# Kernel tuning notes

Measured on AMD Instinct MI355X. Metric: run time of the kernel, lower is better.

The kernel has to match this reference:

```python
import jax, jax.numpy as jnp
import numpy as np
import math

N_LOC = 4096   # spatial locations
N_REP = 128    # replicates n
M_NBR = 48     # conditioning-set size m (fix_m = m_max)
SMOOTH = 1.5


def setup_inputs() -> dict:
    key = jax.random.key(0)
    k1, k2, k3, k4 = jax.random.split(key, 4)
    aug = jax.random.normal(k1, (N_REP, N_LOC, M_NBR + 1), dtype=jnp.float32)
    theta = jax.random.normal(k2, (6,), dtype=jnp.float32) * 0.1
    theta = theta.at[2].set(-2.5)  # slow scaling decay so m_max neighbors are all active
    scales = jax.random.uniform(k3, (N_LOC,), dtype=jnp.float32) + 0.5
    nug_mean = jax.random.uniform(k4, (N_LOC,), dtype=jnp.float32) + 0.5
    batch_idx = jnp.arange(N_LOC, dtype=jnp.int32)
    return {
        "augmented_response": aug,
        "theta": theta,
        "scales": scales,
        "nug_mean": nug_mean,
        "batch_idx": batch_idx,
    }


def _kernel(aug, theta, scales, nug_mean):
    m = aug.shape[-1] - 1
    # x: (n, N, m) -> (N, n, m), nan (no conditioning) -> 0
    x = aug[..., 1 : m + 1]
    x = jnp.where(jnp.isnan(x), 0.0, x)
    x = jnp.transpose(x, (1, 0, 2))  # (N, n, m)
    # scaling_fun(k) = sqrt(exp(-k * exp(theta[2]))), k = 1..m
    ks = jnp.arange(1, m + 1, dtype=aug.dtype)
    scal = jnp.sqrt(jnp.exp(-ks * jnp.exp(theta[2])))  # (m,)
    xs = x * scal  # (N, n, m)
    # linear term: per-location gram matrix (N, n, n)
    lin = jnp.einsum("Nim,Njm->Nij", xs, xs)
    # Matern-1.5 term with unit lengthscale on xs / lenScal
    len_scal = jnp.exp(theta[5]) * math.sqrt(2.0 * SMOOTH)
    xd = xs / len_scal
    sqn = jnp.sum(xd * xd, axis=-1)  # (N, n)
    sq = sqn[:, :, None] + sqn[:, None, :] - 2.0 * jnp.einsum("Nim,Njm->Nij", xd, xd)
    dist = jnp.sqrt(jnp.clip(sq, 0.0))
    sq3d = math.sqrt(3.0) * dist
    matern = (1.0 + sq3d) * jnp.exp(-sq3d)  # nu=1.5 Matern, lengthscale 1
    # sigma_fun per location: exp(log(scales) * theta[4] + theta[3])
    sigma = jnp.exp(jnp.log(scales) * theta[4] + theta[3])  # (N,)
    nonlin = (sigma**2)[:, None, None] * matern
    return (lin + nonlin) / nug_mean[:, None, None]


def reference(augmented_response, theta, scales, nug_mean, batch_idx):
    k = _kernel(augmented_response, theta, scales, nug_mean)  # (N, n, n)
    n = k.shape[-1]
    eye = jnp.eye(n, dtype=k.dtype)
    g = k + eye
    # locations with batch_idx == 0 get identity G
    g = jnp.where((batch_idx == 0)[:, None, None], eye, g)
    g_chol = jnp.linalg.cholesky(g)
    return g, g_chol
```

## Files before the change

kernel.cpp:

```cpp
#include <hip/hip_runtime.h>
#include <math.h>

#define NLOC 4096
#define NREP 128
#define MN   48
#define XSS  49

__global__ __launch_bounds__(256, 2)
void otm_fused(const float* __restrict__ aug,
               const float* __restrict__ theta,
               const float* __restrict__ scales,
               const float* __restrict__ nug_mean,
               const int*   __restrict__ batch_idx,
               float* __restrict__ out_g,
               float* __restrict__ out_l)
{
    __shared__ float xs[NREP * XSS];
    __shared__ float ldiag[NREP];
    __shared__ float scal_s[MN];
    __shared__ float wl[2][8][NREP];
    __shared__ float rs_s[NREP];

    const int loc = blockIdx.x;
    const int tid = threadIdx.x;
    const int ti  = tid >> 4;
    const int tj  = tid & 15;
    const int i0  = ti << 3;
    const int j0  = tj << 3;

    const float th2 = theta[2];
    if (tid < MN) {
        float e2 = expf(th2);
        scal_s[tid] = expf(-0.5f * (float)(tid + 1) * e2);
    }
    __syncthreads();

    for (int idx = tid; idx < NREP * MN; idx += 256) {
        int r = idx / MN;
        int c = idx - r * MN;
        float v = aug[(r * NLOC + loc) * (MN + 1) + 1 + c];
        v = (v != v) ? 0.0f : v;
        xs[r * XSS + c] = v * scal_s[c];
    }
    __syncthreads();

    if (tid < NREP) {
        float s = 0.0f;
        #pragma unroll
        for (int kk = 0; kk < MN; ++kk) {
            float v = xs[tid * XSS + kk];
            s = fmaf(v, v, s);
        }
        ldiag[tid] = s;
    }

    float acc[8][8];
    #pragma unroll
    for (int r = 0; r < 8; ++r)
        #pragma unroll
        for (int c = 0; c < 8; ++c) acc[r][c] = 0.0f;

    for (int kk = 0; kk < MN; ++kk) {
        float a[8], b[8];
        #pragma unroll
        for (int r = 0; r < 8; ++r) a[r] = xs[(i0 + r) * XSS + kk];
        #pragma unroll
        for (int c = 0; c < 8; ++c) b[c] = xs[(j0 + c) * XSS + kk];
        #pragma unroll
        for (int r = 0; r < 8; ++r)
            #pragma unroll
            for (int c = 0; c < 8; ++c)
                acc[r][c] = fmaf(a[r], b[c], acc[r][c]);
    }
    __syncthreads();

    const float s_loc   = scales[loc];
    const float th3 = theta[3], th4 = theta[4], th5 = theta[5];
    const float sig2    = expf(2.0f * fmaf(logf(s_loc), th4, th3));
    const float nug_inv = 1.0f / nug_mean[loc];
    const float ls      = expf(th5) * 1.7320508075688772f;
    const float inv_ls2 = 1.0f / (ls * ls);
    const bool  is0     = (batch_idx[loc] == 0);

    float di[8], dj[8];
    #pragma unroll
    for (int r = 0; r < 8; ++r) di[r] = ldiag[i0 + r];
    #pragma unroll
    for (int c = 0; c < 8; ++c) dj[c] = ldiag[j0 + c];

    float* gout = out_g + (size_t)loc * (NREP * NREP);
    #pragma unroll
    for (int r = 0; r < 8; ++r) {
        const int i = i0 + r;
        #pragma unroll
        for (int h = 0; h < 2; ++h) {
            float tmp[4];
            #pragma unroll
            for (int e = 0; e < 4; ++e) {
                const int c = h * 4 + e;
                const int j = j0 + c;
                float lin = acc[r][c];
                float sq  = (di[r] + dj[c] - 2.0f * lin) * inv_ls2;
                sq = fmaxf(sq, 0.0f);
                float d3  = 1.7320508075688772f * sqrtf(sq);
                float mat = (1.0f + d3) * __expf(-d3);
                float gv  = fmaf(sig2, mat, lin) * nug_inv + ((i == j) ? 1.0f : 0.0f);
                if (is0) gv = (i == j) ? 1.0f : 0.0f;
                acc[r][c] = gv;
                tmp[e] = gv;
            }
            *(float4*)(gout + (size_t)i * NREP + j0 + h * 4) =
                make_float4(tmp[0], tmp[1], tmp[2], tmp[3]);
        }
    }

    for (int p = 0; p < 16; ++p) {
        if (ti == p && tj >= p) {
            const int diagLane = ((p & 3) << 4) | p;
            float rsv[8];
            #pragma unroll
            for (int s = 0; s < 8; ++s) {
                const float piv  = __shfl(acc[s][s], diagLane);
                const float dinv = 1.0f / piv;
                rsv[s] = 1.0f / sqrtf(piv);
                #pragma unroll
                for (int sp = s + 1; sp < 8; ++sp) {
                    const float f = __shfl(acc[sp][s], diagLane) * dinv;
                    #pragma unroll
                    for (int c = 0; c < 8; ++c) {
                        if (c > s) {
                            acc[sp][c] = fmaf(-f, acc[s][c], acc[sp][c]);
                        } else if (tj > p) {
                            acc[sp][c] = fmaf(-f, acc[s][c], acc[sp][c]);
                        }
                    }
                }
            }
            #pragma unroll
            for (int s = 0; s < 8; ++s) {
                *(float4*)&wl[p & 1][s][j0] =
                    make_float4(acc[s][0] * rsv[s], acc[s][1] * rsv[s],
                                acc[s][2] * rsv[s], acc[s][3] * rsv[s]);
                *(float4*)&wl[p & 1][s][j0 + 4] =
                    make_float4(acc[s][4] * rsv[s], acc[s][5] * rsv[s],
                                acc[s][6] * rsv[s], acc[s][7] * rsv[s]);
            }
            if (tj == p) {
                #pragma unroll
                for (int s = 0; s < 8; ++s) rs_s[(p << 3) + s] = rsv[s];
            }
        }
        __syncthreads();

        if (ti > p) {
            const float (*w)[NREP] = wl[p & 1];
            if (tj > p) {
                #pragma unroll 2
                for (int s = 0; s < 8; ++s) {
                    const float4 wiA = *(const float4*)&w[s][i0];
                    const float4 wiB = *(const float4*)&w[s][i0 + 4];
                    const float4 wjA = *(const float4*)&w[s][j0];
                    const float4 wjB = *(const float4*)&w[s][j0 + 4];
                    const float wi[8] = {wiA.x, wiA.y, wiA.z, wiA.w,
                                         wiB.x, wiB.y, wiB.z, wiB.w};
                    const float wj[8] = {wjA.x, wjA.y, wjA.z, wjA.w,
                                         wjB.x, wjB.y, wjB.z, wjB.w};
                    #pragma unroll
                    for (int r = 0; r < 8; ++r)
                        #pragma unroll
                        for (int c = 0; c < 8; ++c)
                            acc[r][c] = fmaf(-wi[r], wj[c], acc[r][c]);
                }
            } else if (tj == p) {
                #pragma unroll
                for (int s = 0; s < 7; ++s) {
                    const float4 wiA = *(const float4*)&w[s][i0];
                    const float4 wiB = *(const float4*)&w[s][i0 + 4];
                    const float wi[8] = {wiA.x, wiA.y, wiA.z, wiA.w,
                                         wiB.x, wiB.y, wiB.z, wiB.w};
                    #pragma unroll
                    for (int c = 0; c < 8; ++c) {
                        if (c > s) {
                            const float wjc = w[s][j0 + c];
                            #pragma unroll
                            for (int r = 0; r < 8; ++r)
                                acc[r][c] = fmaf(-wi[r], wjc, acc[r][c]);
                        }
                    }
                }
            }
        }
    }

    float rsj[8];
    #pragma unroll
    for (int c = 0; c < 8; ++c) rsj[c] = rs_s[j0 + c];

    float* lout = out_l + (size_t)loc * (NREP * NREP);
    #pragma unroll
    for (int r = 0; r < 8; ++r) {
        const int i = i0 + r;
        #pragma unroll
        for (int h = 0; h < 2; ++h) {
            float tmp[4];
            #pragma unroll
            for (int e = 0; e < 4; ++e) {
                const int c = h * 4 + e;
                const int j = j0 + c;
                tmp[e] = (i >= j) ? acc[r][c] * rsj[c] : 0.0f;
            }
            *(float4*)(lout + (size_t)i * NREP + j0 + h * 4) =
                make_float4(tmp[0], tmp[1], tmp[2], tmp[3]);
        }
    }
}

extern "C" void kernel_launch(void* const* d_in, const int* in_sizes, int n_in,
                              void* d_out, int out_size, void* d_ws, size_t ws_size,
                              hipStream_t stream) {
    const float* aug    = (const float*)d_in[0];
    const float* theta  = (const float*)d_in[1];
    const float* scales = (const float*)d_in[2];
    const float* nug    = (const float*)d_in[3];
    const int*   bidx   = (const int*)d_in[4];
    float* g = (float*)d_out;
    float* l = g + (size_t)NLOC * NREP * NREP;
    hipLaunchKernelGGL(otm_fused, dim3(NLOC), dim3(256), 0, stream,
                       aug, theta, scales, nug, bidx, g, l);
}
```

Baseline: 1.209 ms.

## Transpose shared activations to k-major swizzled layout and raise occupancy

The scaled neighbour matrix in shared memory is stored transposed (k-major) with a padded, swizzled row index. This lets the Gram-matrix loop fetch eight rows per operand with two float4 loads instead of eight scalar loads. The Cholesky panel buffer uses the same swizzle to reduce bank conflicts. Launch bounds move from 2 to 4 blocks per CU to hide latency. The odd row stride of 141 floats leaves float4 accesses not 16-byte aligned, and the tighter register budget could cause spills.

```diff
diff --git a/kernel.cpp b/kernel.cpp
--- a/kernel.cpp
+++ b/kernel.cpp
@@ -4,9 +4,12 @@
 #define NLOC 4096
 #define NREP 128
 #define MN   48
-#define XSS  49
-
-__global__ __launch_bounds__(256, 2)
+#define XTS  141
+#define WLS  141
+
+__device__ __forceinline__ int swz(int j) { return j + ((j >> 5) << 2); }
+
+__global__ __launch_bounds__(256, 4)
 void otm_fused(const float* __restrict__ aug,
                const float* __restrict__ theta,
                const float* __restrict__ scales,
@@ -15,10 +18,10 @@
                float* __restrict__ out_g,
                float* __restrict__ out_l)
 {
-    __shared__ float xs[NREP * XSS];
+    __shared__ float xs_t[MN * XTS];
     __shared__ float ldiag[NREP];
     __shared__ float scal_s[MN];
-    __shared__ float wl[2][8][NREP];
+    __shared__ float wl[2][8][WLS];
     __shared__ float rs_s[NREP];
 
     const int loc = blockIdx.x;
@@ -27,6 +30,8 @@
     const int tj  = tid & 15;
     const int i0  = ti << 3;
     const int j0  = tj << 3;
+    const int sa  = swz(i0);
+    const int sb  = swz(j0);
 
     const float th2 = theta[2];
     if (tid < MN) {
@@ -40,15 +45,16 @@
         int c = idx - r * MN;
         float v = aug[(r * NLOC + loc) * (MN + 1) + 1 + c];
         v = (v != v) ? 0.0f : v;
-        xs[r * XSS + c] = v * scal_s[c];
+        xs_t[c * XTS + swz(r)] = v * scal_s[c];
     }
     __syncthreads();
 
     if (tid < NREP) {
+        const int sr = swz(tid);
         float s = 0.0f;
         #pragma unroll
         for (int kk = 0; kk < MN; ++kk) {
-            float v = xs[tid * XSS + kk];
+            float v = xs_t[kk * XTS + sr];
             s = fmaf(v, v, s);
         }
         ldiag[tid] = s;
@@ -60,12 +66,15 @@
         #pragma unroll
         for (int c = 0; c < 8; ++c) acc[r][c] = 0.0f;
 
+    #pragma unroll 4
     for (int kk = 0; kk < MN; ++kk) {
-        float a[8], b[8];
-        #pragma unroll
-        for (int r = 0; r < 8; ++r) a[r] = xs[(i0 + r) * XSS + kk];
-        #pragma unroll
-        for (int c = 0; c < 8; ++c) b[c] = xs[(j0 + c) * XSS + kk];
+        const float* row = &xs_t[kk * XTS];
+        const float4 aA = *(const float4*)(row + sa);
+        const float4 aB = *(const float4*)(row + sa + 4);
+        const float4 bA = *(const float4*)(row + sb);
+        const float4 bB = *(const float4*)(row + sb + 4);
+        const float a[8] = {aA.x, aA.y, aA.z, aA.w, aB.x, aB.y, aB.z, aB.w};
+        const float b[8] = {bA.x, bA.y, bA.z, bA.w, bB.x, bB.y, bB.z, bB.w};
         #pragma unroll
         for (int r = 0; r < 8; ++r)
             #pragma unroll
@@ -138,10 +147,10 @@
             }
             #pragma unroll
             for (int s = 0; s < 8; ++s) {
-                *(float4*)&wl[p & 1][s][j0] =
+                *(float4*)&wl[p & 1][s][sb] =
                     make_float4(acc[s][0] * rsv[s], acc[s][1] * rsv[s],
                                 acc[s][2] * rsv[s], acc[s][3] * rsv[s]);
-                *(float4*)&wl[p & 1][s][j0 + 4] =
+                *(float4*)&wl[p & 1][s][sb + 4] =
                     make_float4(acc[s][4] * rsv[s], acc[s][5] * rsv[s],
                                 acc[s][6] * rsv[s], acc[s][7] * rsv[s]);
             }
@@ -153,14 +162,14 @@
         __syncthreads();
 
         if (ti > p) {
-            const float (*w)[NREP] = wl[p & 1];
+            const float (*w)[WLS] = wl[p & 1];
             if (tj > p) {
                 #pragma unroll 2
                 for (int s = 0; s < 8; ++s) {
-                    const float4 wiA = *(const float4*)&w[s][i0];
-                    const float4 wiB = *(const float4*)&w[s][i0 + 4];
-                    const float4 wjA = *(const float4*)&w[s][j0];
-                    const float4 wjB = *(const float4*)&w[s][j0 + 4];
+                    const float4 wiA = *(const float4*)&w[s][sa];
+                    const float4 wiB = *(const float4*)&w[s][sa + 4];
+                    const float4 wjA = *(const float4*)&w[s][sb];
+                    const float4 wjB = *(const float4*)&w[s][sb + 4];
                     const float wi[8] = {wiA.x, wiA.y, wiA.z, wiA.w,
                                          wiB.x, wiB.y, wiB.z, wiB.w};
                     const float wj[8] = {wjA.x, wjA.y, wjA.z, wjA.w,
@@ -174,14 +183,14 @@
             } else if (tj == p) {
                 #pragma unroll
                 for (int s = 0; s < 7; ++s) {
-                    const float4 wiA = *(const float4*)&w[s][i0];
-                    const float4 wiB = *(const float4*)&w[s][i0 + 4];
+                    const float4 wiA = *(const float4*)&w[s][sa];
+                    const float4 wiB = *(const float4*)&w[s][sa + 4];
                     const float wi[8] = {wiA.x, wiA.y, wiA.z, wiA.w,
                                          wiB.x, wiB.y, wiB.z, wiB.w};
                     #pragma unroll
                     for (int c = 0; c < 8; ++c) {
                         if (c > s) {
-                            const float wjc = w[s][j0 + c];
+                            const float wjc = w[s][sb + c];
                             #pragma unroll
                             for (int r = 0; r < 8; ++r)
                                 acc[r][c] = fmaf(-wi[r], wjc, acc[r][c]);
```

After: 1.381 ms. 14.2% more time.
